# Performance work log

Hardware: AMD Instinct MI355X
Metric: run time of the kernel (lower is better)

## Reference

```python
import jax, jax.numpy as jnp
import numpy as np

N = 4096
NEG_SLOPE = 0.2


def _gat_layer(x, src, dst, W, Wb, a, ab):
    # h = Linear(x); e_ij = a([h_i, h_j]) for each edge; dense softmax over dim=1; ELU
    h = x @ W + Wb                               # [N, D]
    D = h.shape[-1]
    e = h[src] @ a[:D] + h[dst] @ a[D:] + ab     # [E] per-edge attention logits
    n = x.shape[0]
    attn = jnp.full((n, n), -jnp.inf, dtype=x.dtype).at[src, dst].set(e)
    attn = jnp.where(attn > 0, attn, NEG_SLOPE * attn)   # leaky_relu (keeps -inf)
    attn = jax.nn.softmax(attn, axis=1)
    return jax.nn.elu(attn @ h)                  # sigma = ELU


def _multihead(x, src, dst, hW, hWb, ha, hab, oW, oWb, oa, oab):
    # concat=False: mean over head outputs, then out GATLayer
    heads = jax.vmap(lambda W, Wb, a, ab: _gat_layer(x, src, dst, W, Wb, a, ab))(hW, hWb, ha, hab)
    xm = heads.mean(axis=0)
    return _gat_layer(xm, src, dst, oW, oWb, oa, oab)


def setup_inputs() -> dict:
    key = jax.random.key(0)
    ks = jax.random.split(key, 20)
    in_dim, hid, out_dim, H, E = 512, 256, 128, 4, 131072
    x = jax.random.normal(ks[0], (N, in_dim), jnp.float32)
    edge_index = jax.random.randint(ks[1], (2, E), 0, N)
    # force self loops so every softmax row has at least one finite entry
    edge_index = edge_index.at[:, :N].set(jnp.broadcast_to(jnp.arange(N), (2, N)))

    def lin(k, shape, fan_in):
        return jax.random.uniform(k, shape, jnp.float32, -1.0, 1.0) / np.sqrt(fan_in).astype(np.float32)

    return {
        "x": x,
        "edge_index": edge_index,
        # layer 0 (MultiHeadGAT in_dim->hid)
        "l0_hW": lin(ks[2], (H, in_dim, hid), in_dim),
        "l0_hWb": lin(ks[3], (H, hid), in_dim),
        "l0_ha": lin(ks[4], (H, 2 * hid), 2 * hid),
        "l0_hab": lin(ks[5], (H,), 2 * hid),
        "l0_oW": lin(ks[6], (hid, hid), hid),
        "l0_oWb": lin(ks[7], (hid,), hid),
        "l0_oa": lin(ks[8], (2 * hid,), 2 * hid),
        "l0_oab": lin(ks[9], (), 2 * hid),
        # layer 1 (MultiHeadGAT hid->hid)
        "l1_hW": lin(ks[10], (H, hid, hid), hid),
        "l1_hWb": lin(ks[11], (H, hid), hid),
        "l1_ha": lin(ks[12], (H, 2 * hid), 2 * hid),
        "l1_hab": lin(ks[13], (H,), 2 * hid),
        "l1_oW": lin(ks[14], (hid, hid), hid),
        "l1_oWb": lin(ks[15], (hid,), hid),
        "l1_oa": lin(ks[16], (2 * hid,), 2 * hid),
        "l1_oab": lin(ks[17], (), 2 * hid),
        # final Linear(hid -> out_dim)
        "lin_W": lin(ks[18], (hid, out_dim), hid),
        "lin_b": lin(ks[19], (out_dim,), hid),
    }


def reference(x, edge_index, l0_hW, l0_hWb, l0_ha, l0_hab, l0_oW, l0_oWb, l0_oa, l0_oab,
              l1_hW, l1_hWb, l1_ha, l1_hab, l1_oW, l1_oWb, l1_oa, l1_oab, lin_W, lin_b):
    src, dst = edge_index[0], edge_index[1]
    lrelu = lambda v: jnp.where(v > 0, v, NEG_SLOPE * v)
    h = lrelu(_multihead(x, src, dst, l0_hW, l0_hWb, l0_ha, l0_hab, l0_oW, l0_oWb, l0_oa, l0_oab))
    h = lrelu(_multihead(h, src, dst, l1_hW, l1_hWb, l1_ha, l1_hab, l1_oW, l1_oWb, l1_oa, l1_oab))
    return h @ lin_W + lin_b  # [N, out_dim], flatten(1) is a no-op for 2D
```

## Files before the change

### kernel.cpp

```cpp
#include <hip/hip_runtime.h>
#include <hip/hip_bf16.h>
#include <math.h>

#define NEG_SLOPE 0.2f

constexpr int D = 256;
constexpr int HEADS = 4;
constexpr int MAXDEG = 2048;

typedef __attribute__((ext_vector_type(8))) short short8;
typedef __attribute__((ext_vector_type(4))) float floatx4;

__device__ inline unsigned short bf16_hi_trunc(float v) {
  return (unsigned short)(__float_as_uint(v) >> 16);
}
__device__ inline float bf16_tof(unsigned short u) {
  return __uint_as_float(((unsigned int)u) << 16);
}
__device__ inline unsigned short bf16_rn(float v) {
  unsigned int b = __float_as_uint(v);
  b += 0x7fffu + ((b >> 16) & 1u);
  return (unsigned short)(b >> 16);
}
__device__ inline void split2(float v, unsigned short& hi, unsigned short& lo) {
  hi = bf16_hi_trunc(v);
  lo = bf16_rn(v - bf16_tof(hi));
}

__global__ void zero_ints(int* __restrict__ p, int n) {
  int i = blockIdx.x * blockDim.x + threadIdx.x;
  if (i < n) p[i] = 0;
}

__global__ void count_kernel(const int* __restrict__ src, int* __restrict__ cnt, int E) {
  int k = blockIdx.x * blockDim.x + threadIdx.x;
  if (k < E) atomicAdd(&cnt[src[k]], 1);
}

__global__ __launch_bounds__(256) void scan_kernel(const int* __restrict__ cnt,
                                                   int* __restrict__ row_ptr, int Nn) {
  __shared__ int part[256];
  int tid = threadIdx.x;
  int per = Nn >> 8;
  int base = tid * per;
  int local[32];
  int s = 0;
  for (int j = 0; j < per; ++j) { local[j] = cnt[base + j]; s += local[j]; }
  part[tid] = s;
  __syncthreads();
  for (int off = 1; off < 256; off <<= 1) {
    int v = (tid >= off) ? part[tid - off] : 0;
    __syncthreads();
    part[tid] += v;
    __syncthreads();
  }
  int run = part[tid] - s;
  for (int j = 0; j < per; ++j) { row_ptr[base + j] = run; run += local[j]; }
  if (tid == 255) row_ptr[Nn] = run;
}

__global__ void fill_kernel(const int* __restrict__ src, const int* __restrict__ dst,
                            const int* __restrict__ row_ptr, int* __restrict__ cursor,
                            int* __restrict__ col, int E) {
  int k = blockIdx.x * blockDim.x + threadIdx.x;
  if (k < E) {
    int s = src[k];
    int pos = atomicAdd(&cursor[s], 1);
    col[row_ptr[s] + pos] = dst[k];
  }
}

__global__ __launch_bounds__(256) void dedupe_kernel(const int* __restrict__ row_ptr,
                                                     int* __restrict__ col, int Nn) {
  __shared__ int cs[MAXDEG];
  int i = blockIdx.x;
  int start = row_ptr[i];
  int len = row_ptr[i + 1] - start;
  if (len > MAXDEG) len = MAXDEG;
  int tid = threadIdx.x;
  for (int t = tid; t < len; t += 256) cs[t] = col[start + t];
  __syncthreads();
  for (int t = tid; t < len; t += 256) {
    int c = cs[t];
    bool dup = false;
    for (int s2 = 0; s2 < t; ++s2)
      if (cs[s2] == c) { dup = true; break; }
    if (dup) col[start + t] = -1;
  }
}

__global__ __launch_bounds__(256) void prep_kernel(
    const float* __restrict__ x, unsigned short* __restrict__ xhi, unsigned short* __restrict__ xlo,
    int xN4,
    const float* __restrict__ l0hW, unsigned short* __restrict__ l0hHi, unsigned short* __restrict__ l0hLo,
    const float* __restrict__ l1hW, unsigned short* __restrict__ l1hHi, unsigned short* __restrict__ l1hLo,
    const float* __restrict__ l0oW, unsigned short* __restrict__ l0oHi, unsigned short* __restrict__ l0oLo,
    const float* __restrict__ l1oW, unsigned short* __restrict__ l1oHi, unsigned short* __restrict__ l1oLo,
    const float* __restrict__ linW, unsigned short* __restrict__ linHi, unsigned short* __restrict__ linLo) {
  const int b = blockIdx.x;
  const int t = threadIdx.x;
  if (b < 2048) {
    int idx = b * 256 + t;
    if (idx < xN4) {
      float4 v = ((const float4*)x)[idx];
      ushort4 h, l;
      split2(v.x, h.x, l.x);
      split2(v.y, h.y, l.y);
      split2(v.z, h.z, l.z);
      split2(v.w, h.w, l.w);
      ((ushort4*)xhi)[idx] = h;
      ((ushort4*)xlo)[idx] = l;
    }
    return;
  }
  __shared__ float tile[32][33];
  const int tr = t >> 5, tc = t & 31;
  if (b < 2560) {
    const int bi = b - 2048;
    const int kb = bi & 15;
    const int nb = (bi >> 4) & 7;
    const int h = bi >> 7;
    const int K = 512, N = 256;
    const int k0 = kb * 32, n0 = nb * 32;
    const float* B = l0hW + (size_t)h * K * N;
#pragma unroll
    for (int i = 0; i < 4; ++i)
      tile[tr + 8 * i][tc] = B[(size_t)(k0 + tr + 8 * i) * N + (n0 + tc)];
    __syncthreads();
    unsigned short* Thi = l0hHi + (size_t)h * N * K;
    unsigned short* Tlo = l0hLo + (size_t)h * N * K;
#pragma unroll
    for (int i = 0; i < 4; ++i) {
      int n = n0 + tr + 8 * i, k = k0 + tc;
      float v = tile[tc][tr + 8 * i];
      unsigned short hi, lo;
      split2(v, hi, lo);
      Thi[(size_t)n * K + k] = hi;
      Tlo[(size_t)n * K + k] = lo;
    }
    return;
  }
  const int bi = b - 2560;
  const int kb = bi & 7;
  const int nb = (bi >> 3) & 7;
  const int z = bi >> 6;
  const int K = 256;
  const int N = (z == 6) ? 128 : 256;
  const int k0 = kb * 32, n0 = nb * 32;
  if (n0 >= N) return;
  const float* B;
  unsigned short *Thi, *Tlo;
  bool repl4 = false;
  if (z < 4) {
    B = l1hW + (size_t)z * K * 256;
    Thi = l1hHi + (size_t)z * 256 * K;
    Tlo = l1hLo + (size_t)z * 256 * K;
  } else if (z == 4) { B = l0oW; Thi = l0oHi; Tlo = l0oLo; repl4 = true; }
  else if (z == 5)   { B = l1oW; Thi = l1oHi; Tlo = l1oLo; repl4 = true; }
  else               { B = linW; Thi = linHi; Tlo = linLo; }
#pragma unroll
  for (int i = 0; i < 4; ++i)
    tile[tr + 8 * i][tc] = B[(size_t)(k0 + tr + 8 * i) * N + (n0 + tc)];
  __syncthreads();
#pragma unroll
  for (int i = 0; i < 4; ++i) {
    int n = n0 + tr + 8 * i, k = k0 + tc;
    float v = tile[tc][tr + 8 * i];
    if (repl4) {
      unsigned short hi, lo;
      split2(0.25f * v, hi, lo);
#pragma unroll
      for (int h = 0; h < 4; ++h) {
        Thi[(size_t)n * 1024 + h * 256 + k] = hi;
        Tlo[(size_t)n * 1024 + h * 256 + k] = lo;
      }
    } else {
      unsigned short hi, lo;
      split2(v, hi, lo);
      Thi[(size_t)n * K + k] = hi;
      Tlo[(size_t)n * K + k] = lo;
    }
  }
}

__global__ __launch_bounds__(256) void gemm_mfma_split(
    const unsigned short* __restrict__ Ahi, const unsigned short* __restrict__ Alo,
    const unsigned short* __restrict__ Bthi, const unsigned short* __restrict__ Btlo,
    const float* __restrict__ bias, float* __restrict__ C, unsigned short* __restrict__ Cb,
    const float* __restrict__ aptr, float* __restrict__ alphaB, float* __restrict__ betaB,
    int M, int N, int K) {
  constexpr int LSTR = 72;
  __shared__ unsigned short sA[2][64 * LSTR];
  __shared__ unsigned short sB[2][64 * LSTR];
  const int tid = threadIdx.x;
  const int bm = blockIdx.x * 64;
  const int gn = blockIdx.y * 64;
  const int head = (gn) / N;
  const int bn = gn - head * N;

  const int lane = tid & 63;
  const int wv = tid >> 6;
  const int wm = (wv & 1) * 32;
  const int wn = (wv >> 1) * 32;
  const int q = lane >> 4;
  const int l15 = lane & 15;

  floatx4 acc[2][2];
#pragma unroll
  for (int i = 0; i < 2; ++i)
#pragma unroll
    for (int j = 0; j < 2; ++j) acc[i][j] = (floatx4)0.0f;

  for (int k0 = 0; k0 < K; k0 += 64) {
    short8 ra[2][2], rb[2][2];
#pragma unroll
    for (int i = 0; i < 2; ++i) {
      const int c = tid + 256 * i;
      const int row = c >> 3, koff = (c & 7) << 3;
      const size_t aoff = (size_t)(bm + row) * K + k0 + koff;
      const size_t boff = (size_t)(gn + row) * K + k0 + koff;
      ra[0][i] = *(const short8*)(Ahi + aoff);
      ra[1][i] = *(const short8*)(Alo + aoff);
      rb[0][i] = *(const short8*)(Bthi + boff);
      rb[1][i] = *(const short8*)(Btlo + boff);
    }
    __syncthreads();
#pragma unroll
    for (int i = 0; i < 2; ++i) {
      const int c = tid + 256 * i;
      const int row = c >> 3, koff = (c & 7) << 3;
      *(short8*)(&sA[0][row * LSTR + koff]) = ra[0][i];
      *(short8*)(&sA[1][row * LSTR + koff]) = ra[1][i];
      *(short8*)(&sB[0][row * LSTR + koff]) = rb[0][i];
      *(short8*)(&sB[1][row * LSTR + koff]) = rb[1][i];
    }
    __syncthreads();
#pragma unroll
    for (int kc = 0; kc < 2; ++kc) {
      const int ko = kc * 32 + q * 8;
      short8 aH[2], aL[2], bH[2], bL[2];
#pragma unroll
      for (int i = 0; i < 2; ++i) {
        aH[i] = *(const short8*)(&sA[0][(wm + i * 16 + l15) * LSTR + ko]);
        aL[i] = *(const short8*)(&sA[1][(wm + i * 16 + l15) * LSTR + ko]);
        bH[i] = *(const short8*)(&sB[0][(wn + i * 16 + l15) * LSTR + ko]);
        bL[i] = *(const short8*)(&sB[1][(wn + i * 16 + l15) * LSTR + ko]);
      }
#pragma unroll
      for (int i = 0; i < 2; ++i)
#pragma unroll
        for (int j = 0; j < 2; ++j) {
          acc[i][j] = __builtin_amdgcn_mfma_f32_16x16x32_bf16(aH[i], bH[j], acc[i][j], 0, 0, 0);
          acc[i][j] = __builtin_amdgcn_mfma_f32_16x16x32_bf16(aH[i], bL[j], acc[i][j], 0, 0, 0);
          acc[i][j] = __builtin_amdgcn_mfma_f32_16x16x32_bf16(aL[i], bH[j], acc[i][j], 0, 0, 0);
        }
    }
  }
  const size_t cBase = (size_t)head * M * N;
  const int colh0 = bn + wn + l15;
  const int colh1 = colh0 + 16;
  const float bv0 = bias[head * N + colh0];
  const float bv1 = bias[head * N + colh1];
  float as0 = 0.f, as1 = 0.f, ad0 = 0.f, ad1 = 0.f;
  if (aptr) {
    as0 = aptr[head * 2 * N + colh0];
    as1 = aptr[head * 2 * N + colh1];
    ad0 = aptr[head * 2 * N + N + colh0];
    ad1 = aptr[head * 2 * N + N + colh1];
  }
#pragma unroll
  for (int i = 0; i < 2; ++i) {
    const int rowb = bm + wm + i * 16 + q * 4;
#pragma unroll
    for (int r = 0; r < 4; ++r) {
      const float o0 = acc[i][0][r] + bv0;
      const float o1 = acc[i][1][r] + bv1;
      if (Cb) {
        Cb[cBase + (size_t)(rowb + r) * N + colh0] = bf16_rn(o0);
        Cb[cBase + (size_t)(rowb + r) * N + colh1] = bf16_rn(o1);
      } else {
        C[cBase + (size_t)(rowb + r) * N + colh0] = o0;
        C[cBase + (size_t)(rowb + r) * N + colh1] = o1;
      }
      if (aptr) {
        float pa = o0 * as0 + o1 * as1;
        float pb = o0 * ad0 + o1 * ad1;
#pragma unroll
        for (int off = 1; off < 16; off <<= 1) {
          pa += __shfl_xor(pa, off, 64);
          pb += __shfl_xor(pb, off, 64);
        }
        if (l15 == 0) {
          atomicAdd(&alphaB[head * M + rowb + r], pa);
          atomicAdd(&betaB[head * M + rowb + r], pb);
        }
      }
    }
  }
}

__global__ __launch_bounds__(256) void gemm_bias(
    const float* __restrict__ A, const float* __restrict__ B,
    const float* __restrict__ bias, float* __restrict__ C,
    int M, int N, int K) {
  __shared__ float As[16][68];
  __shared__ float Bs[16][68];
  const int tid = threadIdx.x;
  const int bm = blockIdx.x * 64;
  const int gn = blockIdx.y * 64;
  const int head = gn / N;
  const int bn = gn - head * N;
  const float* Bh = B + (size_t)head * K * N;

  const int tx = tid & 15;
  const int ty = tid >> 4;
  const int am = tid >> 2;
  const int ak = (tid & 3) << 2;
  const int bk = tid >> 4;
  const int bn4 = (tid & 15) << 2;

  float acc[4][4] = {};

  for (int k0 = 0; k0 < K; k0 += 16) {
    float4 av = *(const float4*)(A + (size_t)(bm + am) * K + (k0 + ak));
    float4 bv = *(const float4*)(Bh + (size_t)(k0 + bk) * N + (bn + bn4));
    __syncthreads();
    As[ak + 0][am] = av.x;
    As[ak + 1][am] = av.y;
    As[ak + 2][am] = av.z;
    As[ak + 3][am] = av.w;
    *(float4*)(&Bs[bk][bn4]) = bv;
    __syncthreads();
#pragma unroll
    for (int k = 0; k < 16; ++k) {
      float4 aa = *(const float4*)(&As[k][ty << 2]);
      float4 bb = *(const float4*)(&Bs[k][tx << 2]);
      acc[0][0] += aa.x * bb.x; acc[0][1] += aa.x * bb.y; acc[0][2] += aa.x * bb.z; acc[0][3] += aa.x * bb.w;
      acc[1][0] += aa.y * bb.x; acc[1][1] += aa.y * bb.y; acc[1][2] += aa.y * bb.z; acc[1][3] += aa.y * bb.w;
      acc[2][0] += aa.z * bb.x; acc[2][1] += aa.z * bb.y; acc[2][2] += aa.z * bb.z; acc[2][3] += aa.z * bb.w;
      acc[3][0] += aa.w * bb.x; acc[3][1] += aa.w * bb.y; acc[3][2] += aa.w * bb.z; acc[3][3] += aa.w * bb.w;
    }
  }
  float* Ch = C + (size_t)head * M * N;
  const float* bh = bias + (size_t)head * N;
  const int ccol = bn + (tx << 2);
  float4 bias4 = *(const float4*)(bh + ccol);
#pragma unroll
  for (int r = 0; r < 4; ++r) {
    int row = bm + (ty << 2) + r;
    float4 o;
    o.x = acc[r][0] + bias4.x;
    o.y = acc[r][1] + bias4.y;
    o.z = acc[r][2] + bias4.z;
    o.w = acc[r][3] + bias4.w;
    *(float4*)(Ch + (size_t)row * N + ccol) = o;
  }
}

__global__ __launch_bounds__(256) void alphabeta_kernel(
    const float* __restrict__ h, const float* __restrict__ a,
    float* __restrict__ alpha, float* __restrict__ beta, int Nn) {
  __shared__ float reda[4], redb[4];
  const int i = blockIdx.x;
  const int hh = blockIdx.y;
  const int tid = threadIdx.x;
  const int lane = tid & 63, wid = tid >> 6;
  float v = h[((size_t)hh * Nn + i) * D + tid];
  float pa = v * a[hh * 2 * D + tid];
  float pb = v * a[hh * 2 * D + D + tid];
#pragma unroll
  for (int off = 32; off > 0; off >>= 1) {
    pa += __shfl_xor(pa, off, 64);
    pb += __shfl_xor(pb, off, 64);
  }
  if (lane == 0) { reda[wid] = pa; redb[wid] = pb; }
  __syncthreads();
  if (tid == 0) {
    alpha[hh * Nn + i] = reda[0] + reda[1] + reda[2] + reda[3];
    beta[hh * Nn + i] = redb[0] + redb[1] + redb[2] + redb[3];
  }
}

template <int BF16H>
__global__ __launch_bounds__(256) void attn2(
    const float* __restrict__ h, const unsigned short* __restrict__ hB,
    const float* __restrict__ alpha, const float* __restrict__ beta,
    const float* __restrict__ ab, const int* __restrict__ row_ptr,
    const int* __restrict__ col, float* __restrict__ out,
    unsigned short* __restrict__ oHi, unsigned short* __restrict__ oLo,
    int Nn, int H, int mode) {
  const int tid = threadIdx.x;
  const int lane = tid & 63;
  const int wv = tid >> 6;
  const int bx = blockIdx.x;
  const int head = bx % H;
  const int rowblk = bx / H;
  const int i = rowblk * 4 + wv;

  const float* hL = BF16H ? nullptr : (h + (size_t)head * Nn * D + (lane << 2));
  const unsigned short* hLB = BF16H ? (hB + (size_t)head * Nn * D + (lane << 2)) : nullptr;
  const float* betaH = beta + (size_t)head * Nn;
  const float ai = alpha[head * Nn + i] + ab[head];
  const int start = row_ptr[i];
  const int len = row_ptr[i + 1] - start;

  float m = -3.0e38f, s = 0.0f;
  float4 acc0 = make_float4(0.0f, 0.0f, 0.0f, 0.0f);
  float4 acc1 = make_float4(0.0f, 0.0f, 0.0f, 0.0f);

  for (int t0 = 0; t0 < len; t0 += 64) {
    const int t = t0 + lane;
    const int c = (t < len) ? col[start + t] : -1;
    float e = -3.0e38f;
    if (c >= 0) {
      e = ai + betaH[c];
      e = e > 0.0f ? e : NEG_SLOPE * e;
    }
    float cm = e;
#pragma unroll
    for (int off = 32; off > 0; off >>= 1) cm = fmaxf(cm, __shfl_xor(cm, off, 64));
    const float newm = fmaxf(m, cm);
    const float scale = __expf(m - newm);
    const float w = (c >= 0) ? __expf(e - newm) : 0.0f;
    float cs = w;
#pragma unroll
    for (int off = 32; off > 0; off >>= 1) cs += __shfl_xor(cs, off, 64);
    s = s * scale + cs;
    acc0.x *= scale; acc0.y *= scale; acc0.z *= scale; acc0.w *= scale;
    acc1.x *= scale; acc1.y *= scale; acc1.z *= scale; acc1.w *= scale;
    m = newm;

    const int cS = (c >= 0) ? c : 0;
    const int cnt = min(64, len - t0);
    int j = 0;
    if constexpr (BF16H) {
      for (; j + 4 <= cnt; j += 4) {
        const int c0 = __shfl(cS, j);     const float w0 = __shfl(w, j);
        const int c1 = __shfl(cS, j + 1); const float w1 = __shfl(w, j + 1);
        const int c2 = __shfl(cS, j + 2); const float w2 = __shfl(w, j + 2);
        const int c3 = __shfl(cS, j + 3); const float w3 = __shfl(w, j + 3);
        const ushort4 u0 = *(const ushort4*)(hLB + (size_t)c0 * D);
        const ushort4 u1 = *(const ushort4*)(hLB + (size_t)c1 * D);
        const ushort4 u2 = *(const ushort4*)(hLB + (size_t)c2 * D);
        const ushort4 u3 = *(const ushort4*)(hLB + (size_t)c3 * D);
        acc0.x += w0 * bf16_tof(u0.x); acc0.y += w0 * bf16_tof(u0.y);
        acc0.z += w0 * bf16_tof(u0.z); acc0.w += w0 * bf16_tof(u0.w);
        acc1.x += w1 * bf16_tof(u1.x); acc1.y += w1 * bf16_tof(u1.y);
        acc1.z += w1 * bf16_tof(u1.z); acc1.w += w1 * bf16_tof(u1.w);
        acc0.x += w2 * bf16_tof(u2.x); acc0.y += w2 * bf16_tof(u2.y);
        acc0.z += w2 * bf16_tof(u2.z); acc0.w += w2 * bf16_tof(u2.w);
        acc1.x += w3 * bf16_tof(u3.x); acc1.y += w3 * bf16_tof(u3.y);
        acc1.z += w3 * bf16_tof(u3.z); acc1.w += w3 * bf16_tof(u3.w);
      }
      for (; j < cnt; ++j) {
        const int cj = __shfl(cS, j);
        const float wj = __shfl(w, j);
        const ushort4 u = *(const ushort4*)(hLB + (size_t)cj * D);
        acc0.x += wj * bf16_tof(u.x); acc0.y += wj * bf16_tof(u.y);
        acc0.z += wj * bf16_tof(u.z); acc0.w += wj * bf16_tof(u.w);
      }
    } else {
      for (; j + 4 <= cnt; j += 4) {
        const int c0 = __shfl(cS, j);     const float w0 = __shfl(w, j);
        const int c1 = __shfl(cS, j + 1); const float w1 = __shfl(w, j + 1);
        const int c2 = __shfl(cS, j + 2); const float w2 = __shfl(w, j + 2);
        const int c3 = __shfl(cS, j + 3); const float w3 = __shfl(w, j + 3);
        const float4 h0 = *(const float4*)(hL + (size_t)c0 * D);
        const float4 h1 = *(const float4*)(hL + (size_t)c1 * D);
        const float4 h2 = *(const float4*)(hL + (size_t)c2 * D);
        const float4 h3 = *(const float4*)(hL + (size_t)c3 * D);
        acc0.x += w0 * h0.x; acc0.y += w0 * h0.y; acc0.z += w0 * h0.z; acc0.w += w0 * h0.w;
        acc1.x += w1 * h1.x; acc1.y += w1 * h1.y; acc1.z += w1 * h1.z; acc1.w += w1 * h1.w;
        acc0.x += w2 * h2.x; acc0.y += w2 * h2.y; acc0.z += w2 * h2.z; acc0.w += w2 * h2.w;
        acc1.x += w3 * h3.x; acc1.y += w3 * h3.y; acc1.z += w3 * h3.z; acc1.w += w3 * h3.w;
      }
      for (; j < cnt; ++j) {
        const int cj = __shfl(cS, j);
        const float wj = __shfl(w, j);
        const float4 hv = *(const float4*)(hL + (size_t)cj * D);
        acc0.x += wj * hv.x; acc0.y += wj * hv.y;
        acc0.z += wj * hv.z; acc0.w += wj * hv.w;
      }
    }
  }

  const float inv = 1.0f / s;
  float4 v;
  v.x = (acc0.x + acc1.x) * inv; v.y = (acc0.y + acc1.y) * inv;
  v.z = (acc0.z + acc1.z) * inv; v.w = (acc0.w + acc1.w) * inv;
  v.x = v.x > 0.0f ? v.x : expm1f(v.x);
  v.y = v.y > 0.0f ? v.y : expm1f(v.y);
  v.z = v.z > 0.0f ? v.z : expm1f(v.z);
  v.w = v.w > 0.0f ? v.w : expm1f(v.w);

  if (mode == 1 || mode == 3) {
    v.x = v.x > 0.0f ? v.x : NEG_SLOPE * v.x;
    v.y = v.y > 0.0f ? v.y : NEG_SLOPE * v.y;
    v.z = v.z > 0.0f ? v.z : NEG_SLOPE * v.z;
    v.w = v.w > 0.0f ? v.w : NEG_SLOPE * v.w;
    if (mode == 1) {
      *(float4*)(out + (size_t)i * D + (lane << 2)) = v;
    } else {
      ushort4 h4, l4;
      split2(v.x, h4.x, l4.x);
      split2(v.y, h4.y, l4.y);
      split2(v.z, h4.z, l4.z);
      split2(v.w, h4.w, l4.w);
      const size_t q4 = ((size_t)i * D >> 2) + lane;
      ((ushort4*)oHi)[q4] = h4;
      ((ushort4*)oLo)[q4] = l4;
    }
  } else if (mode == 0) {
    if constexpr (BF16H) {
      ushort4 h4, l4;
      split2(v.x, h4.x, l4.x);
      split2(v.y, h4.y, l4.y);
      split2(v.z, h4.z, l4.z);
      split2(v.w, h4.w, l4.w);
      const size_t q4 = ((size_t)i * H + head) * (D / 4) + lane;
      ((ushort4*)oHi)[q4] = h4;
      ((ushort4*)oLo)[q4] = l4;
    } else {
      *(float4*)(out + ((size_t)head * Nn + i) * D + (lane << 2)) = v;
    }
  } else {
    const float invH = 1.0f / (float)H;
    float* o = out + (size_t)i * D + (lane << 2);
    atomicAdd(o + 0, invH * v.x);
    atomicAdd(o + 1, invH * v.y);
    atomicAdd(o + 2, invH * v.z);
    atomicAdd(o + 3, invH * v.w);
  }
}

__global__ __launch_bounds__(256) void mean4_kernel(
    float* __restrict__ hsep, unsigned short* __restrict__ outHi,
    unsigned short* __restrict__ outLo, int total4, int mode) {
  int idx = blockIdx.x * blockDim.x + threadIdx.x;
  if (idx < total4) {
    float4* p = (float4*)hsep;
    float4 a = p[idx], b = p[idx + total4], c = p[idx + 2 * total4], d = p[idx + 3 * total4];
    float4 o;
    o.x = 0.25f * (a.x + b.x + c.x + d.x);
    o.y = 0.25f * (a.y + b.y + c.y + d.y);
    o.z = 0.25f * (a.z + b.z + c.z + d.z);
    o.w = 0.25f * (a.w + b.w + c.w + d.w);
    if (mode == 0) {
      p[idx] = o;
    } else {
      ushort4 h4, l4;
      split2(o.x, h4.x, l4.x);
      split2(o.y, h4.y, l4.y);
      split2(o.z, h4.z, l4.z);
      split2(o.w, h4.w, l4.w);
      ((ushort4*)outHi)[idx] = h4;
      ((ushort4*)outLo)[idx] = l4;
    }
  }
}

__global__ void zero_floats(float* __restrict__ p, int n) {
  int i = blockIdx.x * blockDim.x + threadIdx.x;
  if (i < n) p[i] = 0.0f;
}

extern "C" void kernel_launch(void* const* d_in, const int* in_sizes, int n_in,
                              void* d_out, int out_size, void* d_ws, size_t ws_size,
                              hipStream_t stream) {
  const float* x = (const float*)d_in[0];
  const int* eidx = (const int*)d_in[1];
  const float* l0_hW = (const float*)d_in[2];
  const float* l0_hWb = (const float*)d_in[3];
  const float* l0_ha = (const float*)d_in[4];
  const float* l0_hab = (const float*)d_in[5];
  const float* l0_oW = (const float*)d_in[6];
  const float* l0_oWb = (const float*)d_in[7];
  const float* l0_oa = (const float*)d_in[8];
  const float* l0_oab = (const float*)d_in[9];
  const float* l1_hW = (const float*)d_in[10];
  const float* l1_hWb = (const float*)d_in[11];
  const float* l1_ha = (const float*)d_in[12];
  const float* l1_hab = (const float*)d_in[13];
  const float* l1_oW = (const float*)d_in[14];
  const float* l1_oWb = (const float*)d_in[15];
  const float* l1_oa = (const float*)d_in[16];
  const float* l1_oab = (const float*)d_in[17];
  const float* lin_W = (const float*)d_in[18];
  const float* lin_b = (const float*)d_in[19];

  const int in_dim = 512;
  const int Nn = in_sizes[0] / in_dim;
  const int E = in_sizes[1] / 2;
  const int out_dim = 128;

  char* wsp = (char*)d_ws;
  auto alloc = [&](size_t bytes) {
    char* p = wsp;
    wsp += (bytes + 255) & ~(size_t)255;
    return p;
  };
  const size_t ndBytes = sizeof(float) * (size_t)Nn * D;
  const size_t mfmaNeed = 52000000;
  const bool mfma = ws_size >= mfmaNeed;

  if (mfma) {
    unsigned short* hbufB = (unsigned short*)alloc((size_t)HEADS * Nn * D * 2);
    unsigned short* houtB = (unsigned short*)alloc((size_t)Nn * D * 2);
    unsigned short* aHi   = (unsigned short*)alloc((size_t)Nn * HEADS * D * 2);
    unsigned short* aLo   = (unsigned short*)alloc((size_t)Nn * HEADS * D * 2);
    unsigned short* xhi  = (unsigned short*)alloc((size_t)Nn * in_dim * 2);
    unsigned short* xlo  = (unsigned short*)alloc((size_t)Nn * in_dim * 2);
    unsigned short* x1hi = xhi;
    unsigned short* x1lo = xlo;
    unsigned short* l0hHi = (unsigned short*)alloc((size_t)HEADS * in_dim * D * 2);
    unsigned short* l0hLo = (unsigned short*)alloc((size_t)HEADS * in_dim * D * 2);
    unsigned short* l1hHi = (unsigned short*)alloc((size_t)HEADS * D * D * 2);
    unsigned short* l1hLo = (unsigned short*)alloc((size_t)HEADS * D * D * 2);
    unsigned short* l0oHi = (unsigned short*)alloc((size_t)D * 4 * D * 2);
    unsigned short* l0oLo = (unsigned short*)alloc((size_t)D * 4 * D * 2);
    unsigned short* l1oHi = (unsigned short*)alloc((size_t)D * 4 * D * 2);
    unsigned short* l1oLo = (unsigned short*)alloc((size_t)D * 4 * D * 2);
    unsigned short* linHi = (unsigned short*)alloc((size_t)D * out_dim * 2);
    unsigned short* linLo = (unsigned short*)alloc((size_t)D * out_dim * 2);
    int* cnt     = (int*)alloc(sizeof(int) * Nn);
    int* cursor  = (int*)alloc(sizeof(int) * Nn);
    float* abz   = (float*)alloc(sizeof(float) * 4 * 2 * HEADS * (size_t)Nn);
    int* row_ptr = (int*)alloc(sizeof(int) * (Nn + 1));
    int* col     = (int*)alloc(sizeof(int) * E);
    auto alphaS = [&](int s) { return abz + (size_t)s * 2 * HEADS * Nn; };
    auto betaS  = [&](int s) { return abz + (size_t)s * 2 * HEADS * Nn + HEADS * Nn; };

    const int* src = eidx;
    const int* dst = eidx + E;

    const int zeroN = 2 * Nn + 4 * 2 * HEADS * Nn;
    zero_ints<<<(zeroN + 255) / 256, 256, 0, stream>>>(cnt, zeroN);
    count_kernel<<<(E + 255) / 256, 256, 0, stream>>>(src, cnt, E);
    scan_kernel<<<1, 256, 0, stream>>>(cnt, row_ptr, Nn);
    fill_kernel<<<(E + 255) / 256, 256, 0, stream>>>(src, dst, row_ptr, cursor, col, E);
    dedupe_kernel<<<Nn, 256, 0, stream>>>(row_ptr, col, Nn);

    prep_kernel<<<3008, 256, 0, stream>>>(
        x, xhi, xlo, Nn * in_dim / 4,
        l0_hW, l0hHi, l0hLo, l1_hW, l1hHi, l1hLo,
        l0_oW, l0oHi, l0oLo, l1_oW, l1oHi, l1oLo, lin_W, linHi, linLo);

    gemm_mfma_split<<<dim3(Nn / 64, HEADS * D / 64), 256, 0, stream>>>(
        xhi, xlo, l0hHi, l0hLo, l0_hWb, nullptr, hbufB, l0_ha, alphaS(0), betaS(0), Nn, D, in_dim);
    attn2<1><<<HEADS * (Nn / 4), 256, 0, stream>>>(nullptr, hbufB, alphaS(0), betaS(0), l0_hab,
                                                   row_ptr, col, nullptr, aHi, aLo, Nn, HEADS, 0);
    gemm_mfma_split<<<dim3(Nn / 64, D / 64), 256, 0, stream>>>(
        aHi, aLo, l0oHi, l0oLo, l0_oWb, nullptr, houtB, l0_oa, alphaS(1), betaS(1), Nn, D, HEADS * D);
    attn2<1><<<Nn / 4, 256, 0, stream>>>(nullptr, houtB, alphaS(1), betaS(1), l0_oab,
                                         row_ptr, col, nullptr, x1hi, x1lo, Nn, 1, 3);

    gemm_mfma_split<<<dim3(Nn / 64, HEADS * D / 64), 256, 0, stream>>>(
        x1hi, x1lo, l1hHi, l1hLo, l1_hWb, nullptr, hbufB, l1_ha, alphaS(2), betaS(2), Nn, D, D);
    attn2<1><<<HEADS * (Nn / 4), 256, 0, stream>>>(nullptr, hbufB, alphaS(2), betaS(2), l1_hab,
                                                   row_ptr, col, nullptr, aHi, aLo, Nn, HEADS, 0);
    gemm_mfma_split<<<dim3(Nn / 64, D / 64), 256, 0, stream>>>(
        aHi, aLo, l1oHi, l1oLo, l1_oWb, nullptr, houtB, l1_oa, alphaS(3), betaS(3), Nn, D, HEADS * D);
    attn2<1><<<Nn / 4, 256, 0, stream>>>(nullptr, houtB, alphaS(3), betaS(3), l1_oab,
                                         row_ptr, col, nullptr, x1hi, x1lo, Nn, 1, 3);

    gemm_mfma_split<<<dim3(Nn / 64, out_dim / 64), 256, 0, stream>>>(
        x1hi, x1lo, linHi, linLo, lin_b, (float*)d_out, nullptr, nullptr, nullptr, nullptr, Nn, out_dim, D);
    return;
  }

  const size_t smallBytes = sizeof(float) * 2 * HEADS * (size_t)Nn + sizeof(int) * (3 * Nn + 1 + E) + 4096;
  const bool staged = ws_size >= (8 * ndBytes + 2 * ndBytes + smallBytes + 65536);

  float* hbuf  = (float*)alloc(ndBytes * HEADS);
  float* hsep  = staged ? (float*)alloc(ndBytes * HEADS) : nullptr;
  float* xm    = staged ? hsep : (float*)alloc(ndBytes);
  float* x1    = (float*)alloc(ndBytes);
  float* hout  = (float*)alloc(ndBytes);
  float* alpha = (float*)alloc(sizeof(float) * HEADS * (size_t)Nn);
  float* beta  = (float*)alloc(sizeof(float) * HEADS * (size_t)Nn);
  int* cnt     = (int*)alloc(sizeof(int) * Nn);
  int* cursor  = (int*)alloc(sizeof(int) * Nn);
  int* row_ptr = (int*)alloc(sizeof(int) * (Nn + 1));
  int* col     = (int*)alloc(sizeof(int) * E);

  const int* src = eidx;
  const int* dst = eidx + E;

  zero_ints<<<(2 * Nn + 255) / 256, 256, 0, stream>>>(cnt, 2 * Nn);
  count_kernel<<<(E + 255) / 256, 256, 0, stream>>>(src, cnt, E);
  scan_kernel<<<1, 256, 0, stream>>>(cnt, row_ptr, Nn);
  fill_kernel<<<(E + 255) / 256, 256, 0, stream>>>(src, dst, row_ptr, cursor, col, E);
  dedupe_kernel<<<Nn, 256, 0, stream>>>(row_ptr, col, Nn);

  const int total4 = Nn * D / 4;
  const int meanBlocks = (total4 + 255) / 256;

  gemm_bias<<<dim3(Nn / 64, HEADS * D / 64), 256, 0, stream>>>(x, l0_hW, l0_hWb, hbuf, Nn, D, in_dim);
  alphabeta_kernel<<<dim3(Nn, HEADS), 256, 0, stream>>>(hbuf, l0_ha, alpha, beta, Nn);
  if (staged) {
    attn2<0><<<HEADS * (Nn / 4), 256, 0, stream>>>(hbuf, nullptr, alpha, beta, l0_hab, row_ptr, col, hsep, nullptr, nullptr, Nn, HEADS, 0);
    mean4_kernel<<<meanBlocks, 256, 0, stream>>>(hsep, nullptr, nullptr, total4, 0);
  } else {
    zero_floats<<<(Nn * D + 255) / 256, 256, 0, stream>>>(xm, Nn * D);
    attn2<0><<<HEADS * (Nn / 4), 256, 0, stream>>>(hbuf, nullptr, alpha, beta, l0_hab, row_ptr, col, xm, nullptr, nullptr, Nn, HEADS, 2);
  }
  gemm_bias<<<dim3(Nn / 64, D / 64), 256, 0, stream>>>(xm, l0_oW, l0_oWb, hout, Nn, D, D);
  alphabeta_kernel<<<dim3(Nn, 1), 256, 0, stream>>>(hout, l0_oa, alpha, beta, Nn);
  attn2<0><<<Nn / 4, 256, 0, stream>>>(hout, nullptr, alpha, beta, l0_oab, row_ptr, col, x1, nullptr, nullptr, Nn, 1, 1);

  gemm_bias<<<dim3(Nn / 64, HEADS * D / 64), 256, 0, stream>>>(x1, l1_hW, l1_hWb, hbuf, Nn, D, D);
  alphabeta_kernel<<<dim3(Nn, HEADS), 256, 0, stream>>>(hbuf, l1_ha, alpha, beta, Nn);
  if (staged) {
    attn2<0><<<HEADS * (Nn / 4), 256, 0, stream>>>(hbuf, nullptr, alpha, beta, l1_hab, row_ptr, col, hsep, nullptr, nullptr, Nn, HEADS, 0);
    mean4_kernel<<<meanBlocks, 256, 0, stream>>>(hsep, nullptr, nullptr, total4, 0);
  } else {
    zero_floats<<<(Nn * D + 255) / 256, 256, 0, stream>>>(xm, Nn * D);
    attn2<0><<<HEADS * (Nn / 4), 256, 0, stream>>>(hbuf, nullptr, alpha, beta, l1_hab, row_ptr, col, xm, nullptr, nullptr, Nn, HEADS, 2);
  }
  gemm_bias<<<dim3(Nn / 64, D / 64), 256, 0, stream>>>(xm, l1_oW, l1_oWb, hout, Nn, D, D);
  alphabeta_kernel<<<dim3(Nn, 1), 256, 0, stream>>>(hout, l1_oa, alpha, beta, Nn);
  attn2<0><<<Nn / 4, 256, 0, stream>>>(hout, nullptr, alpha, beta, l1_oab, row_ptr, col, x1, nullptr, nullptr, Nn, 1, 1);

  gemm_bias<<<dim3(Nn / 64, out_dim / 64), 256, 0, stream>>>(x1, lin_W, lin_b, (float*)d_out, Nn, out_dim, D);
}
```

Before: 288.6 us.

## Average head outputs before output projection instead of replicating weights in GEMM

```diff
diff --git a/kernel.cpp b/kernel.cpp
--- a/kernel.cpp
+++ b/kernel.cpp
@@ -150,13 +150,12 @@
   if (n0 >= N) return;
   const float* B;
   unsigned short *Thi, *Tlo;
-  bool repl4 = false;
   if (z < 4) {
     B = l1hW + (size_t)z * K * 256;
     Thi = l1hHi + (size_t)z * 256 * K;
     Tlo = l1hLo + (size_t)z * 256 * K;
-  } else if (z == 4) { B = l0oW; Thi = l0oHi; Tlo = l0oLo; repl4 = true; }
-  else if (z == 5)   { B = l1oW; Thi = l1oHi; Tlo = l1oLo; repl4 = true; }
+  } else if (z == 4) { B = l0oW; Thi = l0oHi; Tlo = l0oLo; }
+  else if (z == 5)   { B = l1oW; Thi = l1oHi; Tlo = l1oLo; }
   else               { B = linW; Thi = linHi; Tlo = linLo; }
 #pragma unroll
   for (int i = 0; i < 4; ++i)
@@ -166,20 +165,10 @@
   for (int i = 0; i < 4; ++i) {
     int n = n0 + tr + 8 * i, k = k0 + tc;
     float v = tile[tc][tr + 8 * i];
-    if (repl4) {
-      unsigned short hi, lo;
-      split2(0.25f * v, hi, lo);
-#pragma unroll
-      for (int h = 0; h < 4; ++h) {
-        Thi[(size_t)n * 1024 + h * 256 + k] = hi;
-        Tlo[(size_t)n * 1024 + h * 256 + k] = lo;
-      }
-    } else {
-      unsigned short hi, lo;
-      split2(v, hi, lo);
-      Thi[(size_t)n * K + k] = hi;
-      Tlo[(size_t)n * K + k] = lo;
-    }
+    unsigned short hi, lo;
+    split2(v, hi, lo);
+    Thi[(size_t)n * K + k] = hi;
+    Tlo[(size_t)n * K + k] = lo;
   }
 }
 
@@ -512,14 +501,13 @@
     }
   } else if (mode == 0) {
     if constexpr (BF16H) {
-      ushort4 h4, l4;
-      split2(v.x, h4.x, l4.x);
-      split2(v.y, h4.y, l4.y);
-      split2(v.z, h4.z, l4.z);
-      split2(v.w, h4.w, l4.w);
-      const size_t q4 = ((size_t)i * H + head) * (D / 4) + lane;
+      ushort4 h4;
+      h4.x = bf16_rn(v.x);
+      h4.y = bf16_rn(v.y);
+      h4.z = bf16_rn(v.z);
+      h4.w = bf16_rn(v.w);
+      const size_t q4 = (((size_t)head * Nn + i) * D >> 2) + lane;
       ((ushort4*)oHi)[q4] = h4;
-      ((ushort4*)oLo)[q4] = l4;
     } else {
       *(float4*)(out + ((size_t)head * Nn + i) * D + (lane << 2)) = v;
     }
@@ -533,9 +521,29 @@
   }
 }
 
+__global__ __launch_bounds__(256) void mean4b_kernel(
+    const unsigned short* __restrict__ hsepB, unsigned short* __restrict__ outHi,
+    unsigned short* __restrict__ outLo, int total4) {
+  int idx = blockIdx.x * blockDim.x + threadIdx.x;
+  if (idx < total4) {
+    const ushort4* p = (const ushort4*)hsepB;
+    ushort4 a = p[idx], b = p[idx + total4], c = p[idx + 2 * total4], d = p[idx + 3 * total4];
+    float ox = 0.25f * (bf16_tof(a.x) + bf16_tof(b.x) + bf16_tof(c.x) + bf16_tof(d.x));
+    float oy = 0.25f * (bf16_tof(a.y) + bf16_tof(b.y) + bf16_tof(c.y) + bf16_tof(d.y));
+    float oz = 0.25f * (bf16_tof(a.z) + bf16_tof(b.z) + bf16_tof(c.z) + bf16_tof(d.z));
+    float ow = 0.25f * (bf16_tof(a.w) + bf16_tof(b.w) + bf16_tof(c.w) + bf16_tof(d.w));
+    ushort4 h4, l4;
+    split2(ox, h4.x, l4.x);
+    split2(oy, h4.y, l4.y);
+    split2(oz, h4.z, l4.z);
+    split2(ow, h4.w, l4.w);
+    ((ushort4*)outHi)[idx] = h4;
+    ((ushort4*)outLo)[idx] = l4;
+  }
+}
+
 __global__ __launch_bounds__(256) void mean4_kernel(
-    float* __restrict__ hsep, unsigned short* __restrict__ outHi,
-    unsigned short* __restrict__ outLo, int total4, int mode) {
+    float* __restrict__ hsep, int total4) {
   int idx = blockIdx.x * blockDim.x + threadIdx.x;
   if (idx < total4) {
     float4* p = (float4*)hsep;
@@ -545,17 +553,7 @@
     o.y = 0.25f * (a.y + b.y + c.y + d.y);
     o.z = 0.25f * (a.z + b.z + c.z + d.z);
     o.w = 0.25f * (a.w + b.w + c.w + d.w);
-    if (mode == 0) {
-      p[idx] = o;
-    } else {
-      ushort4 h4, l4;
-      split2(o.x, h4.x, l4.x);
-      split2(o.y, h4.y, l4.y);
-      split2(o.z, h4.z, l4.z);
-      split2(o.w, h4.w, l4.w);
-      ((ushort4*)outHi)[idx] = h4;
-      ((ushort4*)outLo)[idx] = l4;
-    }
+    p[idx] = o;
   }
 }
 
@@ -606,8 +604,9 @@
   if (mfma) {
     unsigned short* hbufB = (unsigned short*)alloc((size_t)HEADS * Nn * D * 2);
     unsigned short* houtB = (unsigned short*)alloc((size_t)Nn * D * 2);
-    unsigned short* aHi   = (unsigned short*)alloc((size_t)Nn * HEADS * D * 2);
-    unsigned short* aLo   = (unsigned short*)alloc((size_t)Nn * HEADS * D * 2);
+    unsigned short* hsepB = (unsigned short*)alloc((size_t)HEADS * Nn * D * 2);
+    unsigned short* xmhi  = (unsigned short*)alloc((size_t)Nn * D * 2);
+    unsigned short* xmlo  = (unsigned short*)alloc((size_t)Nn * D * 2);
     unsigned short* xhi  = (unsigned short*)alloc((size_t)Nn * in_dim * 2);
     unsigned short* xlo  = (unsigned short*)alloc((size_t)Nn * in_dim * 2);
     unsigned short* x1hi = xhi;
@@ -616,10 +615,10 @@
     unsigned short* l0hLo = (unsigned short*)alloc((size_t)HEADS * in_dim * D * 2);
     unsigned short* l1hHi = (unsigned short*)alloc((size_t)HEADS * D * D * 2);
     unsigned short* l1hLo = (unsigned short*)alloc((size_t)HEADS * D * D * 2);
-    unsigned short* l0oHi = (unsigned short*)alloc((size_t)D * 4 * D * 2);
-    unsigned short* l0oLo = (unsigned short*)alloc((size_t)D * 4 * D * 2);
-    unsigned short* l1oHi = (unsigned short*)alloc((size_t)D * 4 * D * 2);
-    unsigned short* l1oLo = (unsigned short*)alloc((size_t)D * 4 * D * 2);
+    unsigned short* l0oHi = (unsigned short*)alloc((size_t)D * D * 2);
+    unsigned short* l0oLo = (unsigned short*)alloc((size_t)D * D * 2);
+    unsigned short* l1oHi = (unsigned short*)alloc((size_t)D * D * 2);
+    unsigned short* l1oLo = (unsigned short*)alloc((size_t)D * D * 2);
     unsigned short* linHi = (unsigned short*)alloc((size_t)D * out_dim * 2);
     unsigned short* linLo = (unsigned short*)alloc((size_t)D * out_dim * 2);
     int* cnt     = (int*)alloc(sizeof(int) * Nn);
@@ -645,21 +644,26 @@
         l0_hW, l0hHi, l0hLo, l1_hW, l1hHi, l1hLo,
         l0_oW, l0oHi, l0oLo, l1_oW, l1oHi, l1oLo, lin_W, linHi, linLo);
 
+    const int total4 = Nn * D / 4;
+    const int meanBlocks = (total4 + 255) / 256;
+
     gemm_mfma_split<<<dim3(Nn / 64, HEADS * D / 64), 256, 0, stream>>>(
         xhi, xlo, l0hHi, l0hLo, l0_hWb, nullptr, hbufB, l0_ha, alphaS(0), betaS(0), Nn, D, in_dim);
     attn2<1><<<HEADS * (Nn / 4), 256, 0, stream>>>(nullptr, hbufB, alphaS(0), betaS(0), l0_hab,
-                                                   row_ptr, col, nullptr, aHi, aLo, Nn, HEADS, 0);
+                                                   row_ptr, col, nullptr, hsepB, nullptr, Nn, HEADS, 0);
+    mean4b_kernel<<<meanBlocks, 256, 0, stream>>>(hsepB, xmhi, xmlo, total4);
     gemm_mfma_split<<<dim3(Nn / 64, D / 64), 256, 0, stream>>>(
-        aHi, aLo, l0oHi, l0oLo, l0_oWb, nullptr, houtB, l0_oa, alphaS(1), betaS(1), Nn, D, HEADS * D);
+        xmhi, xmlo, l0oHi, l0oLo, l0_oWb, nullptr, houtB, l0_oa, alphaS(1), betaS(1), Nn, D, D);
     attn2<1><<<Nn / 4, 256, 0, stream>>>(nullptr, houtB, alphaS(1), betaS(1), l0_oab,
                                          row_ptr, col, nullptr, x1hi, x1lo, Nn, 1, 3);
 
     gemm_mfma_split<<<dim3(Nn / 64, HEADS * D / 64), 256, 0, stream>>>(
         x1hi, x1lo, l1hHi, l1hLo, l1_hWb, nullptr, hbufB, l1_ha, alphaS(2), betaS(2), Nn, D, D);
     attn2<1><<<HEADS * (Nn / 4), 256, 0, stream>>>(nullptr, hbufB, alphaS(2), betaS(2), l1_hab,
-                                                   row_ptr, col, nullptr, aHi, aLo, Nn, HEADS, 0);
+                                                   row_ptr, col, nullptr, hsepB, nullptr, Nn, HEADS, 0);
+    mean4b_kernel<<<meanBlocks, 256, 0, stream>>>(hsepB, xmhi, xmlo, total4);
     gemm_mfma_split<<<dim3(Nn / 64, D / 64), 256, 0, stream>>>(
-        aHi, aLo, l1oHi, l1oLo, l1_oWb, nullptr, houtB, l1_oa, alphaS(3), betaS(3), Nn, D, HEADS * D);
+        xmhi, xmlo, l1oHi, l1oLo, l1_oWb, nullptr, houtB, l1_oa, alphaS(3), betaS(3), Nn, D, D);
     attn2<1><<<Nn / 4, 256, 0, stream>>>(nullptr, houtB, alphaS(3), betaS(3), l1_oab,
                                          row_ptr, col, nullptr, x1hi, x1lo, Nn, 1, 3);
 
@@ -699,7 +703,7 @@
   alphabeta_kernel<<<dim3(Nn, HEADS), 256, 0, stream>>>(hbuf, l0_ha, alpha, beta, Nn);
   if (staged) {
     attn2<0><<<HEADS * (Nn / 4), 256, 0, stream>>>(hbuf, nullptr, alpha, beta, l0_hab, row_ptr, col, hsep, nullptr, nullptr, Nn, HEADS, 0);
-    mean4_kernel<<<meanBlocks, 256, 0, stream>>>(hsep, nullptr, nullptr, total4, 0);
+    mean4_kernel<<<meanBlocks, 256, 0, stream>>>(hsep, total4);
   } else {
     zero_floats<<<(Nn * D + 255) / 256, 256, 0, stream>>>(xm, Nn * D);
     attn2<0><<<HEADS * (Nn / 4), 256, 0, stream>>>(hbuf, nullptr, alpha, beta, l0_hab, row_ptr, col, xm, nullptr, nullptr, Nn, HEADS, 2);
@@ -712,7 +716,7 @@
   alphabeta_kernel<<<dim3(Nn, HEADS), 256, 0, stream>>>(hbuf, l1_ha, alpha, beta, Nn);
   if (staged) {
     attn2<0><<<HEADS * (Nn / 4), 256, 0, stream>>>(hbuf, nullptr, alpha, beta, l1_hab, row_ptr, col, hsep, nullptr, nullptr, Nn, HEADS, 0);
-    mean4_kernel<<<meanBlocks, 256, 0, stream>>>(hsep, nullptr, nullptr, total4, 0);
+    mean4_kernel<<<meanBlocks, 256, 0, stream>>>(hsep, total4);
   } else {
     zero_floats<<<(Nn * D + 255) / 256, 256, 0, stream>>>(xm, Nn * D);
     attn2<0><<<HEADS * (Nn / 4), 256, 0, stream>>>(hbuf, nullptr, alpha, beta, l1_hab, row_ptr, col, xm, nullptr, nullptr, Nn, HEADS, 2);
```

Measured after the change: 269.8 us. -6.5%, faster.
